# Performance work log

Measured on AMD Instinct MI355X. Metric: run time of the kernel, lower is better.

## Reference

```python
import jax, jax.numpy as jnp
import numpy as np
from jax import lax

H = 128          # lstm hidden size
IN = 128         # time_steps == LSTM input_size
NUM_LAYERS = 3   # num_variables
B = 512          # batch
S = 512          # sequence length


def _lstm_layer(x_tbi, Wih, Whh, bih, bhh):
    """x_tbi: (T, B, in). PyTorch gate order i, f, g, o. Returns (T, B, H), (hT, cT)."""
    T, Bb, _ = x_tbi.shape
    Hh = Whh.shape[1]
    # precompute input contribution to gates outside the scan
    xg = jnp.einsum('tbi,gi->tbg', x_tbi, Wih) + bih + bhh  # (T, B, 4H)

    def step(carry, xg_t):
        h, c = carry
        g = xg_t + h @ Whh.T                                # (B, 4H)
        i, f, gg, o = jnp.split(g, 4, axis=-1)
        c = jax.nn.sigmoid(f) * c + jax.nn.sigmoid(i) * jnp.tanh(gg)
        h = jax.nn.sigmoid(o) * jnp.tanh(c)
        return (h, c), h

    h0 = jnp.zeros((Bb, Hh), x_tbi.dtype)
    c0 = jnp.zeros((Bb, Hh), x_tbi.dtype)
    (hT, cT), ys = lax.scan(step, (h0, c0), xg)
    return ys, (hT, cT)


def setup_inputs() -> dict:
    key = jax.random.key(0)
    ks = jax.random.split(key, 1 + 4 * NUM_LAYERS)
    inp = {"x": jax.random.normal(ks[0], (B, S, IN), dtype=jnp.float32)}
    k = 1.0 / np.sqrt(H)
    ki = 1
    for l in range(NUM_LAYERS):
        in_dim = IN if l == 0 else H
        inp[f"Wih{l}"] = jax.random.uniform(ks[ki], (4 * H, in_dim), jnp.float32, -k, k); ki += 1
        inp[f"Whh{l}"] = jax.random.uniform(ks[ki], (4 * H, H), jnp.float32, -k, k); ki += 1
        inp[f"bih{l}"] = jax.random.uniform(ks[ki], (4 * H,), jnp.float32, -k, k); ki += 1
        inp[f"bhh{l}"] = jax.random.uniform(ks[ki], (4 * H,), jnp.float32, -k, k); ki += 1
    return inp


def reference(x, Wih0, Whh0, bih0, bhh0, Wih1, Whh1, bih1, bhh1, Wih2, Whh2, bih2, bhh2):
    # x: (B, S, IN) -> (S, B, IN), stacked LSTM, output (S, B, H)
    h = jnp.transpose(x, (1, 0, 2))
    params = [(Wih0, Whh0, bih0, bhh0), (Wih1, Whh1, bih1, bhh1), (Wih2, Whh2, bih2, bhh2)]
    for (Wih, Whh, bih, bhh) in params:
        h, _ = _lstm_layer(h, Wih, Whh, bih, bhh)
    # y = output.transpose(1, 2): (S, B, H) -> (S, H, B); dropout is identity in eval
    return jnp.transpose(h, (0, 2, 1))
```

## Files before the change

kernel.cpp:

```cpp
#include <hip/hip_runtime.h>
#include <stdint.h>

#define BATCH 512
#define SEQ   512
#define HID   128
#define BT    16
#define XROW  272
#define XSZ   (BT*XROW)
#define NTILE 32
#define CH    8
#define RING  64
#define FPAD  32
#define SKEW  8

typedef _Float16 half8 __attribute__((ext_vector_type(8)));
typedef float f32x4 __attribute__((ext_vector_type(4)));
typedef unsigned long long u64;

#define BARRIER_LDS() do { \
    asm volatile("s_waitcnt lgkmcnt(0)" ::: "memory"); \
    __builtin_amdgcn_s_barrier(); \
  } while(0)

union UHP { uint32_t u; _Float16 h[2]; };
__device__ __forceinline__ uint32_t pack2f(float a, float b){
  UHP r; r.h[0] = (_Float16)a; r.h[1] = (_Float16)b; return r.u;
}
__device__ __forceinline__ float unpk(uint32_t u, int i){
  UHP r; r.u = u; return (float)r.h[i];
}

__device__ __forceinline__ float rcp_(float x){
#if __has_builtin(__builtin_amdgcn_rcpf)
  return __builtin_amdgcn_rcpf(x);
#else
  return 1.f / x;
#endif
}
__device__ __forceinline__ float exp2_(float x){
#if __has_builtin(__builtin_amdgcn_exp2f)
  return __builtin_amdgcn_exp2f(x);
#else
  return exp2f(x);
#endif
}
__device__ __forceinline__ float sigm(float x){ return rcp_(1.f + exp2_(x * -1.44269504f)); }
__device__ __forceinline__ float tanh_(float x){ return 1.f - 2.f * rcp_(exp2_(x * 2.88539008f) + 1.f); }

__device__ __forceinline__ int aload(const int* p){
  return __hip_atomic_load(p, __ATOMIC_RELAXED, __HIP_MEMORY_SCOPE_AGENT);
}

template<int MODE>
__device__ __forceinline__ void run_layer(
    const float* __restrict__ Wih, const float* __restrict__ Whh,
    const float* __restrict__ bih, const float* __restrict__ bhh,
    const float* __restrict__ x, uint32_t* __restrict__ rin,
    uint32_t* __restrict__ rout, float* __restrict__ y,
    int* src_ready, int* src_done, int* dst_ready, int* dst_done,
    int b0, char* xb, char* hb)
{
  const int tid  = threadIdx.x;
  const int lane = tid & 63;
  const int w    = tid >> 6;
  const int u0   = w * 16;
  const int rm   = lane & 15;
  const int kq   = lane >> 4;

  half8 wih[4][4], whh[4][4];
  #pragma unroll
  for (int g = 0; g < 4; ++g){
    const int grow = g * HID + u0 + rm;
    #pragma unroll
    for (int s = 0; s < 4; ++s){
      const int k = s * 32 + kq * 8;
      const float* si = Wih + (size_t)grow * HID + k;
      const float* sh = Whh + (size_t)grow * HID + k;
      float4 aa = *(const float4*)si, bb = *(const float4*)(si + 4);
      half8 hi;
      hi[0]=(_Float16)aa.x; hi[1]=(_Float16)aa.y; hi[2]=(_Float16)aa.z; hi[3]=(_Float16)aa.w;
      hi[4]=(_Float16)bb.x; hi[5]=(_Float16)bb.y; hi[6]=(_Float16)bb.z; hi[7]=(_Float16)bb.w;
      wih[g][s] = hi;
      aa = *(const float4*)sh; bb = *(const float4*)(sh + 4);
      half8 hh;
      hh[0]=(_Float16)aa.x; hh[1]=(_Float16)aa.y; hh[2]=(_Float16)aa.z; hh[3]=(_Float16)aa.w;
      hh[4]=(_Float16)bb.x; hh[5]=(_Float16)bb.y; hh[6]=(_Float16)bb.z; hh[7]=(_Float16)bb.w;
      whh[g][s] = hh;
    }
  }
  f32x4 bias4[4];
  #pragma unroll
  for (int g = 0; g < 4; ++g)
    #pragma unroll
    for (int r = 0; r < 4; ++r){
      const int row = g * HID + u0 + kq * 4 + r;
      bias4[g][r] = bih[row] + bhh[row];
    }

  const int sb = tid >> 5;
  const int sk = tid & 31;

  auto xaddr = [&](int t){
    return (const float4*)(x + ((size_t)(b0 + sb) * SEQ + t) * HID + sk * 4);
  };
  auto raddr = [&](int t){
    return (u64*)(rin + ((size_t)(t & (RING-1)) * BATCH + b0 + sb) * 64 + sk * 2);
  };

  float4 pfa, pfb;
  u64    pga = 0, pgb = 0;

  int fseen = 0, fpend = 0, dseen = 0;

  if constexpr (MODE != 0){
    fseen = aload(src_ready);
    while (fseen < SKEW){ __builtin_amdgcn_s_sleep(8); fseen = aload(src_ready); }
  }
  if constexpr (MODE == 0){
    float4 v = *xaddr(0);
    uint2 p; p.x = pack2f(v.x, v.y); p.y = pack2f(v.z, v.w);
    *(uint2*)(xb + sb * XROW + sk * 8) = p;
    v = *xaddr(1);
    p.x = pack2f(v.x, v.y); p.y = pack2f(v.z, v.w);
    *(uint2*)(xb + XSZ + sb * XROW + sk * 8) = p;
    pfa = *xaddr(2);
  } else {
    u64 v = __hip_atomic_load(raddr(0), __ATOMIC_RELAXED, __HIP_MEMORY_SCOPE_AGENT);
    *(u64*)(xb + sb * XROW + sk * 8) = v;
    v = __hip_atomic_load(raddr(1), __ATOMIC_RELAXED, __HIP_MEMORY_SCOPE_AGENT);
    *(u64*)(xb + XSZ + sb * XROW + sk * 8) = v;
    pga = __hip_atomic_load(raddr(2), __ATOMIC_RELAXED, __HIP_MEMORY_SCOPE_AGENT);
    fpend = aload(src_ready);
  }
  if (tid < 256)
    *(uint4*)(hb + (tid >> 4) * XROW + (tid & 15) * 16) = make_uint4(0u,0u,0u,0u);
  __syncthreads();

  const int foff = rm * XROW + kq * 16;
  f32x4 a0 = bias4[0], a1 = bias4[1], a2 = bias4[2], a3 = bias4[3];
  #pragma unroll
  for (int s = 0; s < 4; ++s){
    const half8 bf = *(const half8*)(xb + foff + s * 64);
    a0 = __builtin_amdgcn_mfma_f32_16x16x32_f16(wih[0][s], bf, a0, 0, 0, 0);
    a1 = __builtin_amdgcn_mfma_f32_16x16x32_f16(wih[1][s], bf, a1, 0, 0, 0);
    a2 = __builtin_amdgcn_mfma_f32_16x16x32_f16(wih[2][s], bf, a2, 0, 0, 0);
    a3 = __builtin_amdgcn_mfma_f32_16x16x32_f16(wih[3][s], bf, a3, 0, 0, 0);
  }

  f32x4 c4 = {0.f, 0.f, 0.f, 0.f};
  int cur = 0, xr = 1, xw = 2;
  uint2 hp = {0u, 0u};

  for (int t = 0; t < SEQ; ++t){
    char* hbc = hb + cur * XSZ;
    char* hbn = hb + (cur ^ 1) * XSZ;
    char* xbr = xb + xr * XSZ;
    char* xbw = xb + xw * XSZ;
    const int tn = t + 1;

    if (t > 0){
      if constexpr (MODE != 2){
        const u64 hp64 = ((u64)hp.y << 32) | (u64)hp.x;
        u64* p = (u64*)(rout + ((size_t)((t-1) & (RING-1)) * BATCH + b0 + rm) * 64 + (u0 >> 1) + kq * 2);
        __hip_atomic_store(p, hp64, __ATOMIC_RELAXED, __HIP_MEMORY_SCOPE_AGENT);
      } else {
        const size_t yb = ((size_t)(t-1) * HID + u0 + kq * 4) * BATCH + b0 + rm;
        y[yb]             = unpk(hp.x, 0);
        y[yb + BATCH]     = unpk(hp.x, 1);
        y[yb + 2 * BATCH] = unpk(hp.y, 0);
        y[yb + 3 * BATCH] = unpk(hp.y, 1);
      }
    }
    if (tid == 0){
      if constexpr (MODE != 2){
        if (t >= 3)
          __hip_atomic_store(dst_ready, t - 2, __ATOMIC_RELAXED, __HIP_MEMORY_SCOPE_AGENT);
      }
      if constexpr (MODE != 0){
        if ((t & (CH-1)) == 0 && t > 0)
          __hip_atomic_store(src_done, t >> 3, __ATOMIC_RELAXED, __HIP_MEMORY_SCOPE_AGENT);
      }
    }
    if constexpr (MODE != 2){
      if ((t & (CH-1)) == 0 && t >= RING){
        const int need = (t >> 3) - 7;
        if (dseen < need){
          dseen = aload(dst_done);
          while (dseen < need){ __builtin_amdgcn_s_sleep(8); dseen = aload(dst_done); }
        }
      }
    }
    if constexpr (MODE != 0){
      if (fpend > fseen) fseen = fpend;
      fpend = aload(src_ready);
      if (t + 3 < SEQ && fseen < t + 4){
        fseen = aload(src_ready);
        while (fseen < t + 4){ __builtin_amdgcn_s_sleep(2); fseen = aload(src_ready); }
      }
    }
    if (t + 3 < SEQ){
      if constexpr (MODE == 0) pfb = *xaddr(t + 3);
      else pgb = __hip_atomic_load(raddr(t + 3), __ATOMIC_RELAXED, __HIP_MEMORY_SCOPE_AGENT);
    }

    #pragma unroll
    for (int s = 0; s < 4; ++s){
      const half8 bf = *(const half8*)(hbc + foff + s * 64);
      a0 = __builtin_amdgcn_mfma_f32_16x16x32_f16(whh[0][s], bf, a0, 0, 0, 0);
      a1 = __builtin_amdgcn_mfma_f32_16x16x32_f16(whh[1][s], bf, a1, 0, 0, 0);
      a2 = __builtin_amdgcn_mfma_f32_16x16x32_f16(whh[2][s], bf, a2, 0, 0, 0);
      a3 = __builtin_amdgcn_mfma_f32_16x16x32_f16(whh[3][s], bf, a3, 0, 0, 0);
    }

    float hvr[4];
    #pragma unroll
    for (int r = 0; r < 4; ++r){
      const float ii = sigm(a0[r]), ff = sigm(a1[r]);
      const float gg = tanh_(a2[r]), oo = sigm(a3[r]);
      c4[r] = ff * c4[r] + ii * gg;
      hvr[r] = oo * tanh_(c4[r]);
    }
    hp.x = pack2f(hvr[0], hvr[1]);
    hp.y = pack2f(hvr[2], hvr[3]);

    *(uint2*)(hbn + rm * XROW + u0 * 2 + kq * 8) = hp;

    if (t + 2 < SEQ){
      if constexpr (MODE == 0){
        uint2 p; p.x = pack2f(pfa.x, pfa.y); p.y = pack2f(pfa.z, pfa.w);
        *(uint2*)(xbw + sb * XROW + sk * 8) = p;
      } else {
        *(u64*)(xbw + sb * XROW + sk * 8) = pga;
      }
    }

    if (tn < SEQ){
      a0 = bias4[0]; a1 = bias4[1]; a2 = bias4[2]; a3 = bias4[3];
      #pragma unroll
      for (int s = 0; s < 4; ++s){
        const half8 bf = *(const half8*)(xbr + foff + s * 64);
        a0 = __builtin_amdgcn_mfma_f32_16x16x32_f16(wih[0][s], bf, a0, 0, 0, 0);
        a1 = __builtin_amdgcn_mfma_f32_16x16x32_f16(wih[1][s], bf, a1, 0, 0, 0);
        a2 = __builtin_amdgcn_mfma_f32_16x16x32_f16(wih[2][s], bf, a2, 0, 0, 0);
        a3 = __builtin_amdgcn_mfma_f32_16x16x32_f16(wih[3][s], bf, a3, 0, 0, 0);
      }
    }

    BARRIER_LDS();
    pfa = pfb; pga = pgb;
    xr = (xr == 2) ? 0 : xr + 1;
    xw = (xw == 2) ? 0 : xw + 1;
    cur ^= 1;
  }

  if constexpr (MODE != 2){
    const u64 hp64 = ((u64)hp.y << 32) | (u64)hp.x;
    u64* p = (u64*)(rout + ((size_t)((SEQ-1) & (RING-1)) * BATCH + b0 + rm) * 64 + (u0 >> 1) + kq * 2);
    __hip_atomic_store(p, hp64, __ATOMIC_RELAXED, __HIP_MEMORY_SCOPE_AGENT);
  } else {
    const size_t yb = ((size_t)(SEQ-1) * HID + u0 + kq * 4) * BATCH + b0 + rm;
    y[yb]             = unpk(hp.x, 0);
    y[yb + BATCH]     = unpk(hp.x, 1);
    y[yb + 2 * BATCH] = unpk(hp.y, 0);
    y[yb + 3 * BATCH] = unpk(hp.y, 1);
  }
  __syncthreads();
  if (tid == 0){
    if constexpr (MODE != 2)
      __hip_atomic_store(dst_ready, SEQ, __ATOMIC_RELAXED, __HIP_MEMORY_SCOPE_AGENT);
    if constexpr (MODE != 0)
      __hip_atomic_store(src_done, SEQ / CH, __ATOMIC_RELAXED, __HIP_MEMORY_SCOPE_AGENT);
  }
}

__global__ __launch_bounds__(512, 2) void lstm_pipe(
    const float* W0i, const float* W0h, const float* b0i, const float* b0h,
    const float* W1i, const float* W1h, const float* b1i, const float* b1h,
    const float* W2i, const float* W2h, const float* b2i, const float* b2h,
    const float* x, float* y, uint32_t* ring, int* flags)
{
  const int layer = blockIdx.x >> 5;
  const int tile  = blockIdx.x & 31;
  const int b0    = tile * BT;

  __shared__ char smem[5 * XSZ];
  char* xb = smem;
  char* hb = smem + 3 * XSZ;

  uint32_t* r0 = ring;
  uint32_t* r1 = ring + (size_t)RING * BATCH * 64;

  int* p0 = flags + (0 * NTILE + tile) * FPAD;
  int* p1 = flags + (1 * NTILE + tile) * FPAD;
  int* c0 = flags + (2 * NTILE + tile) * FPAD;
  int* c1 = flags + (3 * NTILE + tile) * FPAD;

  if (layer == 0){
    run_layer<0>(W0i, W0h, b0i, b0h, x, nullptr, r0, nullptr,
                 nullptr, nullptr, p0, c0, b0, xb, hb);
  } else if (layer == 1){
    run_layer<1>(W1i, W1h, b1i, b1h, nullptr, r0, r1, nullptr,
                 p0, c0, p1, c1, b0, xb, hb);
  } else {
    run_layer<2>(W2i, W2h, b2i, b2h, nullptr, r1, nullptr, y,
                 p1, c1, nullptr, nullptr, b0, xb, hb);
  }
}

extern "C" void kernel_launch(void* const* d_in, const int* in_sizes, int n_in,
                              void* d_out, int out_size, void* d_ws, size_t ws_size,
                              hipStream_t stream) {
  const float* x    = (const float*)d_in[0];
  const float* Wih0 = (const float*)d_in[1];
  const float* Whh0 = (const float*)d_in[2];
  const float* bih0 = (const float*)d_in[3];
  const float* bhh0 = (const float*)d_in[4];
  const float* Wih1 = (const float*)d_in[5];
  const float* Whh1 = (const float*)d_in[6];
  const float* bih1 = (const float*)d_in[7];
  const float* bhh1 = (const float*)d_in[8];
  const float* Wih2 = (const float*)d_in[9];
  const float* Whh2 = (const float*)d_in[10];
  const float* bih2 = (const float*)d_in[11];
  const float* bhh2 = (const float*)d_in[12];

  float* out = (float*)d_out;
  uint32_t* ring = (uint32_t*)d_ws;
  const size_t ring_bytes = (size_t)2 * RING * BATCH * 64 * 4;
  int* flags = (int*)((char*)d_ws + ring_bytes);

  hipMemsetAsync(flags, 0, 4 * NTILE * FPAD * sizeof(int), stream);

  dim3 grid(3 * NTILE), block(512);
  lstm_pipe<<<grid, block, 0, stream>>>(
      Wih0, Whh0, bih0, bhh0, Wih1, Whh1, bih1, bhh1, Wih2, Whh2, bih2, bhh2,
      x, out, ring, flags);
}
```

Baseline: 661.1 us.

## Process two batch tiles per block to interleave independent recurrences

Each workgroup now handles two 16-row batch tiles (A and B) instead of one, which halves the grid to 48 blocks. The MFMA chains and gate math of the two tiles are interleaved so that each tile's work fills the other's dependency latency in the serial recurrence. Weights held in registers are shared between the two tiles. The cost is that each timestep does twice the work per block, register pressure rises with the extra accumulators and cell state, LDS use doubles, and fewer CUs are used.

```diff
diff --git a/kernel.cpp b/kernel.cpp
--- a/kernel.cpp
+++ b/kernel.cpp
@@ -7,7 +7,7 @@
 #define BT    16
 #define XROW  272
 #define XSZ   (BT*XROW)
-#define NTILE 32
+#define NPAIR 16
 #define CH    8
 #define RING  64
 #define FPAD  32
@@ -58,7 +58,8 @@
     const float* __restrict__ x, uint32_t* __restrict__ rin,
     uint32_t* __restrict__ rout, float* __restrict__ y,
     int* src_ready, int* src_done, int* dst_ready, int* dst_done,
-    int b0, char* xb, char* hb)
+    int b0A, int b0B,
+    char* xbA, char* hbA, char* xbB, char* hbB)
 {
   const int tid  = threadIdx.x;
   const int lane = tid & 63;
@@ -100,15 +101,21 @@
   const int sb = tid >> 5;
   const int sk = tid & 31;
 
-  auto xaddr = [&](int t){
-    return (const float4*)(x + ((size_t)(b0 + sb) * SEQ + t) * HID + sk * 4);
+  auto xaddrA = [&](int t){
+    return (const float4*)(x + ((size_t)(b0A + sb) * SEQ + t) * HID + sk * 4);
   };
-  auto raddr = [&](int t){
-    return (u64*)(rin + ((size_t)(t & (RING-1)) * BATCH + b0 + sb) * 64 + sk * 2);
+  auto xaddrB = [&](int t){
+    return (const float4*)(x + ((size_t)(b0B + sb) * SEQ + t) * HID + sk * 4);
   };
-
-  float4 pfa, pfb;
-  u64    pga = 0, pgb = 0;
+  auto raddrA = [&](int t){
+    return (u64*)(rin + ((size_t)(t & (RING-1)) * BATCH + b0A + sb) * 64 + sk * 2);
+  };
+  auto raddrB = [&](int t){
+    return (u64*)(rin + ((size_t)(t & (RING-1)) * BATCH + b0B + sb) * 64 + sk * 2);
+  };
+
+  float4 pfaA, pfbA, pfaB, pfbB;
+  u64    pgaA = 0, pgbA = 0, pgaB = 0, pgbB = 0;
 
   int fseen = 0, fpend = 0, dseen = 0;
 
@@ -117,58 +124,86 @@
     while (fseen < SKEW){ __builtin_amdgcn_s_sleep(8); fseen = aload(src_ready); }
   }
   if constexpr (MODE == 0){
-    float4 v = *xaddr(0);
+    float4 v = *xaddrA(0);
     uint2 p; p.x = pack2f(v.x, v.y); p.y = pack2f(v.z, v.w);
-    *(uint2*)(xb + sb * XROW + sk * 8) = p;
-    v = *xaddr(1);
+    *(uint2*)(xbA + sb * XROW + sk * 8) = p;
+    v = *xaddrB(0);
     p.x = pack2f(v.x, v.y); p.y = pack2f(v.z, v.w);
-    *(uint2*)(xb + XSZ + sb * XROW + sk * 8) = p;
-    pfa = *xaddr(2);
+    *(uint2*)(xbB + sb * XROW + sk * 8) = p;
+    v = *xaddrA(1);
+    p.x = pack2f(v.x, v.y); p.y = pack2f(v.z, v.w);
+    *(uint2*)(xbA + XSZ + sb * XROW + sk * 8) = p;
+    v = *xaddrB(1);
+    p.x = pack2f(v.x, v.y); p.y = pack2f(v.z, v.w);
+    *(uint2*)(xbB + XSZ + sb * XROW + sk * 8) = p;
+    pfaA = *xaddrA(2);
+    pfaB = *xaddrB(2);
   } else {
-    u64 v = __hip_atomic_load(raddr(0), __ATOMIC_RELAXED, __HIP_MEMORY_SCOPE_AGENT);
-    *(u64*)(xb + sb * XROW + sk * 8) = v;
-    v = __hip_atomic_load(raddr(1), __ATOMIC_RELAXED, __HIP_MEMORY_SCOPE_AGENT);
-    *(u64*)(xb + XSZ + sb * XROW + sk * 8) = v;
-    pga = __hip_atomic_load(raddr(2), __ATOMIC_RELAXED, __HIP_MEMORY_SCOPE_AGENT);
+    u64 v = __hip_atomic_load(raddrA(0), __ATOMIC_RELAXED, __HIP_MEMORY_SCOPE_AGENT);
+    *(u64*)(xbA + sb * XROW + sk * 8) = v;
+    v = __hip_atomic_load(raddrB(0), __ATOMIC_RELAXED, __HIP_MEMORY_SCOPE_AGENT);
+    *(u64*)(xbB + sb * XROW + sk * 8) = v;
+    v = __hip_atomic_load(raddrA(1), __ATOMIC_RELAXED, __HIP_MEMORY_SCOPE_AGENT);
+    *(u64*)(xbA + XSZ + sb * XROW + sk * 8) = v;
+    v = __hip_atomic_load(raddrB(1), __ATOMIC_RELAXED, __HIP_MEMORY_SCOPE_AGENT);
+    *(u64*)(xbB + XSZ + sb * XROW + sk * 8) = v;
+    pgaA = __hip_atomic_load(raddrA(2), __ATOMIC_RELAXED, __HIP_MEMORY_SCOPE_AGENT);
+    pgaB = __hip_atomic_load(raddrB(2), __ATOMIC_RELAXED, __HIP_MEMORY_SCOPE_AGENT);
     fpend = aload(src_ready);
   }
-  if (tid < 256)
-    *(uint4*)(hb + (tid >> 4) * XROW + (tid & 15) * 16) = make_uint4(0u,0u,0u,0u);
+  if (tid < 256){
+    *(uint4*)(hbA + (tid >> 4) * XROW + (tid & 15) * 16) = make_uint4(0u,0u,0u,0u);
+    *(uint4*)(hbB + (tid >> 4) * XROW + (tid & 15) * 16) = make_uint4(0u,0u,0u,0u);
+  }
   __syncthreads();
 
   const int foff = rm * XROW + kq * 16;
-  f32x4 a0 = bias4[0], a1 = bias4[1], a2 = bias4[2], a3 = bias4[3];
+  f32x4 aA0 = bias4[0], aA1 = bias4[1], aA2 = bias4[2], aA3 = bias4[3];
+  f32x4 aB0 = bias4[0], aB1 = bias4[1], aB2 = bias4[2], aB3 = bias4[3];
   #pragma unroll
   for (int s = 0; s < 4; ++s){
-    const half8 bf = *(const half8*)(xb + foff + s * 64);
-    a0 = __builtin_amdgcn_mfma_f32_16x16x32_f16(wih[0][s], bf, a0, 0, 0, 0);
-    a1 = __builtin_amdgcn_mfma_f32_16x16x32_f16(wih[1][s], bf, a1, 0, 0, 0);
-    a2 = __builtin_amdgcn_mfma_f32_16x16x32_f16(wih[2][s], bf, a2, 0, 0, 0);
-    a3 = __builtin_amdgcn_mfma_f32_16x16x32_f16(wih[3][s], bf, a3, 0, 0, 0);
-  }
-
-  f32x4 c4 = {0.f, 0.f, 0.f, 0.f};
+    const half8 bfA = *(const half8*)(xbA + foff + s * 64);
+    const half8 bfB = *(const half8*)(xbB + foff + s * 64);
+    aA0 = __builtin_amdgcn_mfma_f32_16x16x32_f16(wih[0][s], bfA, aA0, 0, 0, 0);
+    aB0 = __builtin_amdgcn_mfma_f32_16x16x32_f16(wih[0][s], bfB, aB0, 0, 0, 0);
+    aA1 = __builtin_amdgcn_mfma_f32_16x16x32_f16(wih[1][s], bfA, aA1, 0, 0, 0);
+    aB1 = __builtin_amdgcn_mfma_f32_16x16x32_f16(wih[1][s], bfB, aB1, 0, 0, 0);
+    aA2 = __builtin_amdgcn_mfma_f32_16x16x32_f16(wih[2][s], bfA, aA2, 0, 0, 0);
+    aB2 = __builtin_amdgcn_mfma_f32_16x16x32_f16(wih[2][s], bfB, aB2, 0, 0, 0);
+    aA3 = __builtin_amdgcn_mfma_f32_16x16x32_f16(wih[3][s], bfA, aA3, 0, 0, 0);
+    aB3 = __builtin_amdgcn_mfma_f32_16x16x32_f16(wih[3][s], bfB, aB3, 0, 0, 0);
+  }
+
+  f32x4 cA = {0.f,0.f,0.f,0.f}, cB = {0.f,0.f,0.f,0.f};
   int cur = 0, xr = 1, xw = 2;
-  uint2 hp = {0u, 0u};
+  uint2 hpA = {0u,0u}, hpB = {0u,0u};
 
   for (int t = 0; t < SEQ; ++t){
-    char* hbc = hb + cur * XSZ;
-    char* hbn = hb + (cur ^ 1) * XSZ;
-    char* xbr = xb + xr * XSZ;
-    char* xbw = xb + xw * XSZ;
+    char* hbcA = hbA + cur * XSZ;        char* hbcB = hbB + cur * XSZ;
+    char* hbnA = hbA + (cur ^ 1) * XSZ;  char* hbnB = hbB + (cur ^ 1) * XSZ;
+    char* xbrA = xbA + xr * XSZ;         char* xbrB = xbB + xr * XSZ;
+    char* xbwA = xbA + xw * XSZ;         char* xbwB = xbB + xw * XSZ;
     const int tn = t + 1;
 
     if (t > 0){
       if constexpr (MODE != 2){
-        const u64 hp64 = ((u64)hp.y << 32) | (u64)hp.x;
-        u64* p = (u64*)(rout + ((size_t)((t-1) & (RING-1)) * BATCH + b0 + rm) * 64 + (u0 >> 1) + kq * 2);
-        __hip_atomic_store(p, hp64, __ATOMIC_RELAXED, __HIP_MEMORY_SCOPE_AGENT);
+        const u64 hA = ((u64)hpA.y << 32) | (u64)hpA.x;
+        const u64 hB = ((u64)hpB.y << 32) | (u64)hpB.x;
+        u64* pA = (u64*)(rout + ((size_t)((t-1) & (RING-1)) * BATCH + b0A + rm) * 64 + (u0 >> 1) + kq * 2);
+        u64* pB = (u64*)(rout + ((size_t)((t-1) & (RING-1)) * BATCH + b0B + rm) * 64 + (u0 >> 1) + kq * 2);
+        __hip_atomic_store(pA, hA, __ATOMIC_RELAXED, __HIP_MEMORY_SCOPE_AGENT);
+        __hip_atomic_store(pB, hB, __ATOMIC_RELAXED, __HIP_MEMORY_SCOPE_AGENT);
       } else {
-        const size_t yb = ((size_t)(t-1) * HID + u0 + kq * 4) * BATCH + b0 + rm;
-        y[yb]             = unpk(hp.x, 0);
-        y[yb + BATCH]     = unpk(hp.x, 1);
-        y[yb + 2 * BATCH] = unpk(hp.y, 0);
-        y[yb + 3 * BATCH] = unpk(hp.y, 1);
+        const size_t ybA = ((size_t)(t-1) * HID + u0 + kq * 4) * BATCH + b0A + rm;
+        const size_t ybB = ((size_t)(t-1) * HID + u0 + kq * 4) * BATCH + b0B + rm;
+        y[ybA]             = unpk(hpA.x, 0);
+        y[ybA + BATCH]     = unpk(hpA.x, 1);
+        y[ybA + 2 * BATCH] = unpk(hpA.y, 0);
+        y[ybA + 3 * BATCH] = unpk(hpA.y, 1);
+        y[ybB]             = unpk(hpB.x, 0);
+        y[ybB + BATCH]     = unpk(hpB.x, 1);
+        y[ybB + 2 * BATCH] = unpk(hpB.y, 0);
+        y[ybB + 3 * BATCH] = unpk(hpB.y, 1);
       }
     }
     if (tid == 0){
@@ -199,70 +234,105 @@
       }
     }
     if (t + 3 < SEQ){
-      if constexpr (MODE == 0) pfb = *xaddr(t + 3);
-      else pgb = __hip_atomic_load(raddr(t + 3), __ATOMIC_RELAXED, __HIP_MEMORY_SCOPE_AGENT);
+      if constexpr (MODE == 0){
+        pfbA = *xaddrA(t + 3);
+        pfbB = *xaddrB(t + 3);
+      } else {
+        pgbA = __hip_atomic_load(raddrA(t + 3), __ATOMIC_RELAXED, __HIP_MEMORY_SCOPE_AGENT);
+        pgbB = __hip_atomic_load(raddrB(t + 3), __ATOMIC_RELAXED, __HIP_MEMORY_SCOPE_AGENT);
+      }
     }
 
     #pragma unroll
     for (int s = 0; s < 4; ++s){
-      const half8 bf = *(const half8*)(hbc + foff + s * 64);
-      a0 = __builtin_amdgcn_mfma_f32_16x16x32_f16(whh[0][s], bf, a0, 0, 0, 0);
-      a1 = __builtin_amdgcn_mfma_f32_16x16x32_f16(whh[1][s], bf, a1, 0, 0, 0);
-      a2 = __builtin_amdgcn_mfma_f32_16x16x32_f16(whh[2][s], bf, a2, 0, 0, 0);
-      a3 = __builtin_amdgcn_mfma_f32_16x16x32_f16(whh[3][s], bf, a3, 0, 0, 0);
-    }
-
-    float hvr[4];
-    #pragma unroll
-    for (int r = 0; r < 4; ++r){
-      const float ii = sigm(a0[r]), ff = sigm(a1[r]);
-      const float gg = tanh_(a2[r]), oo = sigm(a3[r]);
-      c4[r] = ff * c4[r] + ii * gg;
-      hvr[r] = oo * tanh_(c4[r]);
-    }
-    hp.x = pack2f(hvr[0], hvr[1]);
-    hp.y = pack2f(hvr[2], hvr[3]);
-
-    *(uint2*)(hbn + rm * XROW + u0 * 2 + kq * 8) = hp;
+      const half8 bfA = *(const half8*)(hbcA + foff + s * 64);
+      const half8 bfB = *(const half8*)(hbcB + foff + s * 64);
+      aA0 = __builtin_amdgcn_mfma_f32_16x16x32_f16(whh[0][s], bfA, aA0, 0, 0, 0);
+      aB0 = __builtin_amdgcn_mfma_f32_16x16x32_f16(whh[0][s], bfB, aB0, 0, 0, 0);
+      aA1 = __builtin_amdgcn_mfma_f32_16x16x32_f16(whh[1][s], bfA, aA1, 0, 0, 0);
+      aB1 = __builtin_amdgcn_mfma_f32_16x16x32_f16(whh[1][s], bfB, aB1, 0, 0, 0);
+      aA2 = __builtin_amdgcn_mfma_f32_16x16x32_f16(whh[2][s], bfA, aA2, 0, 0, 0);
+      aB2 = __builtin_amdgcn_mfma_f32_16x16x32_f16(whh[2][s], bfB, aB2, 0, 0, 0);
+      aA3 = __builtin_amdgcn_mfma_f32_16x16x32_f16(whh[3][s], bfA, aA3, 0, 0, 0);
+      aB3 = __builtin_amdgcn_mfma_f32_16x16x32_f16(whh[3][s], bfB, aB3, 0, 0, 0);
+    }
+
+    {
+      float hvA[4], hvB[4];
+      #pragma unroll
+      for (int r = 0; r < 4; ++r){
+        const float iiA = sigm(aA0[r]), ffA = sigm(aA1[r]);
+        const float ggA = tanh_(aA2[r]), ooA = sigm(aA3[r]);
+        const float iiB = sigm(aB0[r]), ffB = sigm(aB1[r]);
+        const float ggB = tanh_(aB2[r]), ooB = sigm(aB3[r]);
+        cA[r] = ffA * cA[r] + iiA * ggA;
+        cB[r] = ffB * cB[r] + iiB * ggB;
+        hvA[r] = ooA * tanh_(cA[r]);
+        hvB[r] = ooB * tanh_(cB[r]);
+      }
+      hpA.x = pack2f(hvA[0], hvA[1]);  hpA.y = pack2f(hvA[2], hvA[3]);
+      hpB.x = pack2f(hvB[0], hvB[1]);  hpB.y = pack2f(hvB[2], hvB[3]);
+    }
+
+    *(uint2*)(hbnA + rm * XROW + u0 * 2 + kq * 8) = hpA;
+    *(uint2*)(hbnB + rm * XROW + u0 * 2 + kq * 8) = hpB;
 
     if (t + 2 < SEQ){
       if constexpr (MODE == 0){
-        uint2 p; p.x = pack2f(pfa.x, pfa.y); p.y = pack2f(pfa.z, pfa.w);
-        *(uint2*)(xbw + sb * XROW + sk * 8) = p;
+        uint2 p;
+        p.x = pack2f(pfaA.x, pfaA.y); p.y = pack2f(pfaA.z, pfaA.w);
+        *(uint2*)(xbwA + sb * XROW + sk * 8) = p;
+        p.x = pack2f(pfaB.x, pfaB.y); p.y = pack2f(pfaB.z, pfaB.w);
+        *(uint2*)(xbwB + sb * XROW + sk * 8) = p;
       } else {
-        *(u64*)(xbw + sb * XROW + sk * 8) = pga;
+        *(u64*)(xbwA + sb * XROW + sk * 8) = pgaA;
+        *(u64*)(xbwB + sb * XROW + sk * 8) = pgaB;
       }
     }
 
     if (tn < SEQ){
-      a0 = bias4[0]; a1 = bias4[1]; a2 = bias4[2]; a3 = bias4[3];
+      aA0 = bias4[0]; aA1 = bias4[1]; aA2 = bias4[2]; aA3 = bias4[3];
+      aB0 = bias4[0]; aB1 = bias4[1]; aB2 = bias4[2]; aB3 = bias4[3];
       #pragma unroll
       for (int s = 0; s < 4; ++s){
-        const half8 bf = *(const half8*)(xbr + foff + s * 64);
-        a0 = __builtin_amdgcn_mfma_f32_16x16x32_f16(wih[0][s], bf, a0, 0, 0, 0);
-        a1 = __builtin_amdgcn_mfma_f32_16x16x32_f16(wih[1][s], bf, a1, 0, 0, 0);
-        a2 = __builtin_amdgcn_mfma_f32_16x16x32_f16(wih[2][s], bf, a2, 0, 0, 0);
-        a3 = __builtin_amdgcn_mfma_f32_16x16x32_f16(wih[3][s], bf, a3, 0, 0, 0);
+        const half8 bfA = *(const half8*)(xbrA + foff + s * 64);
+        const half8 bfB = *(const half8*)(xbrB + foff + s * 64);
+        aA0 = __builtin_amdgcn_mfma_f32_16x16x32_f16(wih[0][s], bfA, aA0, 0, 0, 0);
+        aB0 = __builtin_amdgcn_mfma_f32_16x16x32_f16(wih[0][s], bfB, aB0, 0, 0, 0);
+        aA1 = __builtin_amdgcn_mfma_f32_16x16x32_f16(wih[1][s], bfA, aA1, 0, 0, 0);
+        aB1 = __builtin_amdgcn_mfma_f32_16x16x32_f16(wih[1][s], bfB, aB1, 0, 0, 0);
+        aA2 = __builtin_amdgcn_mfma_f32_16x16x32_f16(wih[2][s], bfA, aA2, 0, 0, 0);
+        aB2 = __builtin_amdgcn_mfma_f32_16x16x32_f16(wih[2][s], bfB, aB2, 0, 0, 0);
+        aA3 = __builtin_amdgcn_mfma_f32_16x16x32_f16(wih[3][s], bfA, aA3, 0, 0, 0);
+        aB3 = __builtin_amdgcn_mfma_f32_16x16x32_f16(wih[3][s], bfB, aB3, 0, 0, 0);
       }
     }
 
     BARRIER_LDS();
-    pfa = pfb; pga = pgb;
+    pfaA = pfbA; pfaB = pfbB; pgaA = pgbA; pgaB = pgbB;
     xr = (xr == 2) ? 0 : xr + 1;
     xw = (xw == 2) ? 0 : xw + 1;
     cur ^= 1;
   }
 
   if constexpr (MODE != 2){
-    const u64 hp64 = ((u64)hp.y << 32) | (u64)hp.x;
-    u64* p = (u64*)(rout + ((size_t)((SEQ-1) & (RING-1)) * BATCH + b0 + rm) * 64 + (u0 >> 1) + kq * 2);
-    __hip_atomic_store(p, hp64, __ATOMIC_RELAXED, __HIP_MEMORY_SCOPE_AGENT);
+    const u64 hA = ((u64)hpA.y << 32) | (u64)hpA.x;
+    const u64 hB = ((u64)hpB.y << 32) | (u64)hpB.x;
+    u64* pA = (u64*)(rout + ((size_t)((SEQ-1) & (RING-1)) * BATCH + b0A + rm) * 64 + (u0 >> 1) + kq * 2);
+    u64* pB = (u64*)(rout + ((size_t)((SEQ-1) & (RING-1)) * BATCH + b0B + rm) * 64 + (u0 >> 1) + kq * 2);
+    __hip_atomic_store(pA, hA, __ATOMIC_RELAXED, __HIP_MEMORY_SCOPE_AGENT);
+    __hip_atomic_store(pB, hB, __ATOMIC_RELAXED, __HIP_MEMORY_SCOPE_AGENT);
   } else {
-    const size_t yb = ((size_t)(SEQ-1) * HID + u0 + kq * 4) * BATCH + b0 + rm;
-    y[yb]             = unpk(hp.x, 0);
-    y[yb + BATCH]     = unpk(hp.x, 1);
-    y[yb + 2 * BATCH] = unpk(hp.y, 0);
-    y[yb + 3 * BATCH] = unpk(hp.y, 1);
+    const size_t ybA = ((size_t)(SEQ-1) * HID + u0 + kq * 4) * BATCH + b0A + rm;
+    const size_t ybB = ((size_t)(SEQ-1) * HID + u0 + kq * 4) * BATCH + b0B + rm;
+    y[ybA]             = unpk(hpA.x, 0);
+    y[ybA + BATCH]     = unpk(hpA.x, 1);
+    y[ybA + 2 * BATCH] = unpk(hpA.y, 0);
+    y[ybA + 3 * BATCH] = unpk(hpA.y, 1);
+    y[ybB]             = unpk(hpB.x, 0);
+    y[ybB + BATCH]     = unpk(hpB.x, 1);
+    y[ybB + 2 * BATCH] = unpk(hpB.y, 0);
+    y[ybB + 3 * BATCH] = unpk(hpB.y, 1);
   }
   __syncthreads();
   if (tid == 0){
@@ -279,31 +349,34 @@
     const float* W2i, const float* W2h, const float* b2i, const float* b2h,
     const float* x, float* y, uint32_t* ring, int* flags)
 {
-  const int layer = blockIdx.x >> 5;
-  const int tile  = blockIdx.x & 31;
-  const int b0    = tile * BT;
-
-  __shared__ char smem[5 * XSZ];
-  char* xb = smem;
-  char* hb = smem + 3 * XSZ;
+  const int layer = blockIdx.x / NPAIR;
+  const int pair  = blockIdx.x % NPAIR;
+  const int b0A   = pair * 2 * BT;
+  const int b0B   = b0A + BT;
+
+  __shared__ char smem[10 * XSZ];
+  char* xbA = smem;
+  char* hbA = smem + 3 * XSZ;
+  char* xbB = smem + 5 * XSZ;
+  char* hbB = smem + 8 * XSZ;
 
   uint32_t* r0 = ring;
   uint32_t* r1 = ring + (size_t)RING * BATCH * 64;
 
-  int* p0 = flags + (0 * NTILE + tile) * FPAD;
-  int* p1 = flags + (1 * NTILE + tile) * FPAD;
-  int* c0 = flags + (2 * NTILE + tile) * FPAD;
-  int* c1 = flags + (3 * NTILE + tile) * FPAD;
+  int* p0 = flags + (0 * NPAIR + pair) * FPAD;
+  int* p1 = flags + (1 * NPAIR + pair) * FPAD;
+  int* c0 = flags + (2 * NPAIR + pair) * FPAD;
+  int* c1 = flags + (3 * NPAIR + pair) * FPAD;
 
   if (layer == 0){
     run_layer<0>(W0i, W0h, b0i, b0h, x, nullptr, r0, nullptr,
-                 nullptr, nullptr, p0, c0, b0, xb, hb);
+                 nullptr, nullptr, p0, c0, b0A, b0B, xbA, hbA, xbB, hbB);
   } else if (layer == 1){
     run_layer<1>(W1i, W1h, b1i, b1h, nullptr, r0, r1, nullptr,
-                 p0, c0, p1, c1, b0, xb, hb);
+                 p0, c0, p1, c1, b0A, b0B, xbA, hbA, xbB, hbB);
   } else {
     run_layer<2>(W2i, W2h, b2i, b2h, nullptr, r1, nullptr, y,
-                 p1, c1, nullptr, nullptr, b0, xb, hb);
+                 p1, c1, nullptr, nullptr, b0A, b0B, xbA, hbA, xbB, hbB);
   }
 }
 
@@ -329,9 +402,9 @@
   const size_t ring_bytes = (size_t)2 * RING * BATCH * 64 * 4;
   int* flags = (int*)((char*)d_ws + ring_bytes);
 
-  hipMemsetAsync(flags, 0, 4 * NTILE * FPAD * sizeof(int), stream);
-
-  dim3 grid(3 * NTILE), block(512);
+  hipMemsetAsync(flags, 0, 4 * NPAIR * FPAD * sizeof(int), stream);
+
+  dim3 grid(3 * NPAIR), block(512);
   lstm_pipe<<<grid, block, 0, stream>>>(
       Wih0, Whh0, bih0, bhh0, Wih1, Whh1, bih1, bhh1, Wih2, Whh2, bih2, bhh2,
       x, out, ring, flags);
```

Measured after the change: 1.255 ms. +89.8%, slower.
